# Kernel optimization log

Hardware: AMD Instinct MI355X
Metric: run time of the kernel (lower is better)

Reference implementation:

```python
import jax, jax.numpy as jnp
import numpy as np

B, S, D = 4, 8192, 512


def setup_inputs() -> dict:
    key = jax.random.key(0)
    k1, k2, k3 = jax.random.split(key, 3)
    input_real = jax.random.normal(k1, (B, S, D), dtype=jnp.float32)
    input_imag = jax.random.normal(k2, (B, S, D), dtype=jnp.float32)
    weight = jax.random.uniform(k3, (B, S), dtype=jnp.float32)
    return {"input_real": input_real, "input_imag": input_imag, "weight": weight}


def reference(input_real, input_imag, weight):
    # Original: sum_s w[b,s] * (r_s r_s^T + i_s i_s^T)  and  sum_s w[b,s] * (i_s r_s^T - r_s i_s^T).
    # Algebraically equal to weighted Gram GEMMs X^T diag(w) Y; avoids the [B,S,D,D] intermediate.
    def wgram(x, y):
        # [B,S,D] x [B,S] x [B,S,D] -> [B,D,D]
        return jnp.einsum('bsd,bs,bse->bde', x, weight, y)

    output_r = wgram(input_real, input_real) + wgram(input_imag, input_imag)
    output_i = wgram(input_imag, input_real) - wgram(input_real, input_imag)
    return (output_r, output_i)
```

## Files before the change

### kernel.cpp

```cpp
#include <hip/hip_runtime.h>
#include <cstdint>
#include <cstddef>

#define NB 4
#define NS 8192
#define ND 512
#define NP 1024
#define BK 32

typedef __bf16 bf16x8 __attribute__((ext_vector_type(8)));
typedef float f32x4 __attribute__((ext_vector_type(4)));

union FragU { uint4 u; bf16x8 h; };

__device__ __forceinline__ void gload16(const void* g, void* l) {
  __builtin_amdgcn_global_load_lds(
      (const __attribute__((address_space(1))) unsigned int*)g,
      (__attribute__((address_space(3))) unsigned int*)l, 16, 0, 0);
}

__global__ __launch_bounds__(256)
void k_prep(const float* __restrict__ R, const float* __restrict__ I,
            const float* __restrict__ W, unsigned short* __restrict__ Yt) {
  __shared__ unsigned T[64][34];
  const int t   = threadIdx.x;
  const int blk = blockIdx.x;
  const int sb  = blk & 127;
  const int pb  = (blk >> 7) & 15;
  const int b   = blk >> 11;
  const float* src = (pb < 8) ? R : I;
  const int col0 = (pb & 7) * 64;
  const int s0 = sb * 64;
  const int c2 = t & 15;
  const int rp = t >> 4;
#pragma unroll
  for (int i = 0; i < 2; ++i) {
    const int r  = rp + 16 * i;
    const int sa = s0 + 2 * r;
    const float swa = sqrtf(W[b * NS + sa]);
    const float swb = sqrtf(W[b * NS + sa + 1]);
    const float4 va = *(const float4*)(src + (size_t)(b * NS + sa) * ND + col0 + c2 * 4);
    const float4 vb = *(const float4*)(src + (size_t)(b * NS + sa + 1) * ND + col0 + c2 * 4);
    unsigned p0, p1, p2, p3;
    asm("v_cvt_pk_bf16_f32 %0, %1, %2" : "=v"(p0) : "v"(va.x * swa), "v"(vb.x * swb));
    asm("v_cvt_pk_bf16_f32 %0, %1, %2" : "=v"(p1) : "v"(va.y * swa), "v"(vb.y * swb));
    asm("v_cvt_pk_bf16_f32 %0, %1, %2" : "=v"(p2) : "v"(va.z * swa), "v"(vb.z * swb));
    asm("v_cvt_pk_bf16_f32 %0, %1, %2" : "=v"(p3) : "v"(va.w * swa), "v"(vb.w * swb));
    T[c2 * 4 + 0][r] = p0;
    T[c2 * 4 + 1][r] = p1;
    T[c2 * 4 + 2][r] = p2;
    T[c2 * 4 + 3][r] = p3;
  }
  __syncthreads();
  const int sc = t & 7;
  const int d0 = t >> 3;
#pragma unroll
  for (int i = 0; i < 2; ++i) {
    const int d = d0 + 32 * i;
    uint4 o;
    o.x = T[d][sc * 4 + 0];
    o.y = T[d][sc * 4 + 1];
    o.z = T[d][sc * 4 + 2];
    o.w = T[d][sc * 4 + 3];
    *(uint4*)(Yt + (size_t)(b * NP + pb * 64 + d) * NS + s0 + sc * 8) = o;
  }
}

__global__ __launch_bounds__(256, 2)
void k_gemm(const unsigned short* __restrict__ Yt, float* __restrict__ part) {
  __shared__ uint4 lds4[4096];
  char* lds = (char*)lds4;
  static const int TMp[10] = {0,1,1,2,2,2,3,3,3,3};
  static const int TNp[10] = {0,0,1,0,1,2,0,1,2,3};
  const int j  = blockIdx.x;
  const int g0 = j * 20;
  const int g1 = g0 + 20;
  const int p0 = g0 >> 8;
  const int p1 = (g1 - 1) >> 8;
  const int t = threadIdx.x;
  const int l = t & 63, w = t >> 6;

  const int cj = l & 7, jj = l >> 3;
  const int ec = cj ^ jj;
  const int rbase = w * 16 + 2 * jj + (ec >> 2);
  const int colo  = (ec & 3) * 8;
  int dstoff[8];
#pragma unroll
  for (int u = 0; u < 8; ++u) dstoff[u] = (u >> 1) * 8192 + (u & 1) * 4096 + w * 1024;

  const int gfr = l >> 4, e_ = l & 1, q = (l >> 1) & 7;
  const int ibase = ((l & 15) >> 1) * 128 + ((64 * e_ + 16 * gfr) ^ (q << 4));
  const int wm = w & 1, wn = w >> 1;
  const int mfb = wm * 4096, nfb = wn * 4096;
  const int lr = (l >> 4) * 4, lc = l & 15;

  for (int seg = 0; seg < 2; ++seg) {
    int pos, k0, ns;
    if (seg == 0) {
      pos = p0; k0 = g0 & 255;
      ns = 256 - k0; if (ns > 20) ns = 20;
    } else {
      if (p1 == p0) break;
      pos = p1; k0 = 0; ns = g1 & 255;
    }
    const int b = pos / 10, p = pos % 10;
    const int tm = TMp[p], tn = TNp[p];
    const int prow[4] = { tm * 128, 512 + tm * 128, tn * 128, 512 + tn * 128 };
    const unsigned short* gsrc[8];
#pragma unroll
    for (int u = 0; u < 8; ++u)
      gsrc[u] = Yt + (size_t)(b * NP + prow[u >> 1] + (u & 1) * 64 + rbase) * NS
                + (size_t)k0 * BK + colo;

    f32x4 accr[4][4], acci[4][4];
    const f32x4 zz = {0.f, 0.f, 0.f, 0.f};
#pragma unroll
    for (int a = 0; a < 4; ++a)
#pragma unroll
      for (int c = 0; c < 4; ++c) { accr[a][c] = zz; acci[a][c] = zz; }

#pragma unroll
    for (int u = 0; u < 8; ++u) { gload16(gsrc[u], lds + dstoff[u]); gsrc[u] += BK; }
    __builtin_amdgcn_sched_barrier(0);
    asm volatile("s_waitcnt vmcnt(0)" ::: "memory");
    __builtin_amdgcn_s_barrier();

    int cur = 0;
    for (int ks = 0; ks < ns; ++ks) {
      const int cbase = cur * 32768;
      if (ks + 1 < ns) {
        const int nbase = cbase ^ 32768;
#pragma unroll
        for (int u = 0; u < 8; ++u) { gload16(gsrc[u], lds + nbase + dstoff[u]); gsrc[u] += BK; }
        __builtin_amdgcn_sched_barrier(0);
        asm volatile("s_waitcnt vmcnt(8)" ::: "memory");
      } else {
        asm volatile("s_waitcnt vmcnt(0)" ::: "memory");
      }
      __builtin_amdgcn_s_barrier();

      FragU ar[4], ai[4];
#pragma unroll
      for (int mf = 0; mf < 4; ++mf) {
        ar[mf].u = *(const uint4*)(lds + cbase +        mfb + mf * 1024 + ibase);
        ai[mf].u = *(const uint4*)(lds + cbase + 8192 + mfb + mf * 1024 + ibase);
      }
      __builtin_amdgcn_s_setprio(1);
#pragma unroll
      for (int nf = 0; nf < 4; ++nf) {
        FragU br, bi, bin;
        br.u = *(const uint4*)(lds + cbase + 16384 + nfb + nf * 1024 + ibase);
        bi.u = *(const uint4*)(lds + cbase + 24576 + nfb + nf * 1024 + ibase);
        bin.u.x = bi.u.x ^ 0x80008000u;
        bin.u.y = bi.u.y ^ 0x80008000u;
        bin.u.z = bi.u.z ^ 0x80008000u;
        bin.u.w = bi.u.w ^ 0x80008000u;
#pragma unroll
        for (int mf = 0; mf < 4; ++mf) {
          accr[mf][nf] = __builtin_amdgcn_mfma_f32_16x16x32_bf16(ar[mf].h, br.h,  accr[mf][nf], 0, 0, 0);
          accr[mf][nf] = __builtin_amdgcn_mfma_f32_16x16x32_bf16(ai[mf].h, bi.h,  accr[mf][nf], 0, 0, 0);
          acci[mf][nf] = __builtin_amdgcn_mfma_f32_16x16x32_bf16(ai[mf].h, br.h,  acci[mf][nf], 0, 0, 0);
          acci[mf][nf] = __builtin_amdgcn_mfma_f32_16x16x32_bf16(ar[mf].h, bin.h, acci[mf][nf], 0, 0, 0);
        }
      }
      __builtin_amdgcn_s_setprio(0);
      __builtin_amdgcn_s_barrier();
      cur ^= 1;
    }

    const int slot = (seg == 0) ? j : (512 + pos);
    const size_t baser = (size_t)slot * 32768;
    const size_t basei = baser + 16384;
#pragma unroll
    for (int mf = 0; mf < 4; ++mf)
#pragma unroll
      for (int nf = 0; nf < 4; ++nf)
#pragma unroll
        for (int r = 0; r < 4; ++r) {
          const int mi = wm * 64 + mf * 16 + lr + r;
          const int ni = wn * 64 + nf * 16 + lc;
          part[baser + (size_t)mi * 128 + ni] = accr[mf][nf][r];
          part[basei + (size_t)mi * 128 + ni] = acci[mf][nf][r];
        }
  }
}

__global__ __launch_bounds__(256)
void k_reduce(const float* __restrict__ part, float* __restrict__ out) {
  static const int TMp[10] = {0,1,1,2,2,2,3,3,3,3};
  static const int TNp[10] = {0,0,1,0,1,2,0,1,2,3};
  const int idx = blockIdx.x * 256 + threadIdx.x;
  const int ni = idx & 127;
  const int mi = (idx >> 7) & 127;
  const int o  = (idx >> 14) & 1;
  const int P  = idx >> 15;
  const int jlo = (256 * P + 19) / 20;
  const int jhi = (256 * P + 255) / 20;
  const size_t off = (size_t)o * 16384 + (size_t)mi * 128 + ni;
  float a = 0.f;
  for (int s = jlo; s <= jhi; ++s)
    a += part[(size_t)s * 32768 + off];
  if ((256 * P) % 20)
    a += part[(size_t)(512 + P) * 32768 + off];
  const int b = P / 10, p = P % 10;
  const int d = TMp[p] * 128 + mi;
  const int e = TNp[p] * 128 + ni;
  out[(size_t)o * 1048576 + (size_t)b * 262144 + (size_t)d * 512 + e] = a;
}

__global__ __launch_bounds__(256)
void k_mirror(float* __restrict__ out) {
  __shared__ float T[64][65];
  static const int UM[6] = {0,0,0,1,1,2};
  static const int UN[6] = {1,2,3,2,3,3};
  const int m = blockIdx.x;
  const int sub = m & 3;
  const int b   = (m >> 2) & 3;
  const int o   = (m >> 4) & 1;
  const int u   = m >> 5;
  const int d0 = UM[u] * 128 + (sub & 1) * 64;
  const int e0 = UN[u] * 128 + ((sub >> 1) & 1) * 64;
  const float sign = o ? -1.f : 1.f;
  float* base = out + (size_t)o * 1048576 + (size_t)b * 262144;
  const int t  = threadIdx.x;
  const int c4 = (t & 15) * 4;
  const int r0 = t >> 4;
#pragma unroll
  for (int i = 0; i < 4; ++i) {
    const int r = r0 + i * 16;
    const float4 v = *(const float4*)(base + (size_t)(e0 + r) * 512 + d0 + c4);
    T[c4 + 0][r] = v.x; T[c4 + 1][r] = v.y;
    T[c4 + 2][r] = v.z; T[c4 + 3][r] = v.w;
  }
  __syncthreads();
#pragma unroll
  for (int i = 0; i < 4; ++i) {
    const int r = r0 + i * 16;
    float4 wv;
    wv.x = sign * T[r][c4 + 0]; wv.y = sign * T[r][c4 + 1];
    wv.z = sign * T[r][c4 + 2]; wv.w = sign * T[r][c4 + 3];
    *(float4*)(base + (size_t)(d0 + r) * 512 + e0 + c4) = wv;
  }
}

__global__ __launch_bounds__(256)
void k_fallback(const float* __restrict__ R, const float* __restrict__ I,
                const float* __restrict__ W, float* __restrict__ out) {
  __shared__ float Rd[64][32], Id[64][32], Re[64][32], Ie[64][32];
  const int blk = blockIdx.x;
  const int et = blk & 15, dt = (blk >> 4) & 15, b = blk >> 8;
  const int d0 = dt * 32, e0 = et * 32;
  const int t = threadIdx.x;
  const int dd = t >> 3;
  const int ee0 = (t & 7) * 4;
  float ar[4] = {0,0,0,0}, ai[4] = {0,0,0,0};
  for (int s0 = 0; s0 < NS; s0 += 64) {
#pragma unroll
    for (int k = 0; k < 8; ++k) {
      const int idx = t + k * 256;
      const int row = idx >> 5, col = idx & 31;
      const float sw = sqrtf(W[b * NS + s0 + row]);
      const size_t gr = (size_t)(b * NS + s0 + row) * ND;
      Rd[row][col] = R[gr + d0 + col] * sw;
      Id[row][col] = I[gr + d0 + col] * sw;
      Re[row][col] = R[gr + e0 + col] * sw;
      Ie[row][col] = I[gr + e0 + col] * sw;
    }
    __syncthreads();
    for (int s = 0; s < 64; ++s) {
      const float rd = Rd[s][dd], id = Id[s][dd];
#pragma unroll
      for (int jx = 0; jx < 4; ++jx) {
        const float re = Re[s][ee0 + jx], ie = Ie[s][ee0 + jx];
        ar[jx] += rd * re + id * ie;
        ai[jx] += id * re - rd * ie;
      }
    }
    __syncthreads();
  }
  const size_t ob = (size_t)b * 262144;
#pragma unroll
  for (int jx = 0; jx < 4; ++jx) {
    out[          ob + (size_t)(d0 + dd) * 512 + e0 + ee0 + jx] = ar[jx];
    out[1048576 + ob + (size_t)(d0 + dd) * 512 + e0 + ee0 + jx] = ai[jx];
  }
}

extern "C" void kernel_launch(void* const* d_in, const int* in_sizes, int n_in,
                              void* d_out, int out_size, void* d_ws, size_t ws_size,
                              hipStream_t stream) {
  const float* R = (const float*)d_in[0];
  const float* I = (const float*)d_in[1];
  const float* W = (const float*)d_in[2];
  float* out = (float*)d_out;
  const size_t ytBytes   = (size_t)NB * NP * NS * 2;
  const size_t partBytes = (size_t)552 * 32768 * 4;

  if (ws_size < ytBytes + partBytes) {
    k_fallback<<<dim3(NB * 16 * 16), dim3(256), 0, stream>>>(R, I, W, out);
    return;
  }

  unsigned short* Yt = (unsigned short*)d_ws;
  float* part = (float*)((char*)d_ws + ytBytes);

  k_prep<<<dim3(NB * 16 * 128), dim3(256), 0, stream>>>(R, I, W, Yt);
  k_gemm<<<dim3(512), dim3(256), 0, stream>>>(Yt, part);
  k_reduce<<<dim3(5120), dim3(256), 0, stream>>>(part, out);
  k_mirror<<<dim3(192), dim3(256), 0, stream>>>(out);
}
```

Before: 232.6 us.

## Use 8-wave GEMM blocks, swizzle block order, vectorize partial reduction

The GEMM kernel now runs 512 threads per block. Each wave owns a 32x64 sub-tile instead of 64x64, which halves its accumulator registers and the global-to-LDS loads per thread. Block indices are remapped so that consecutive blocks land on strided work chunks, likely for better spread across XCDs or cache locality. The reduction kernel now reads and writes float4 instead of scalars and launches a quarter as many blocks. The trade-off is more LDS fragment reads per MFMA for each wave and higher register pressure from the launch_bounds(512,4) target.

```diff
diff --git a/kernel.cpp b/kernel.cpp
--- a/kernel.cpp
+++ b/kernel.cpp
@@ -66,13 +66,14 @@
   }
 }
 
-__global__ __launch_bounds__(256, 2)
+__global__ __launch_bounds__(512, 4)
 void k_gemm(const unsigned short* __restrict__ Yt, float* __restrict__ part) {
   __shared__ uint4 lds4[4096];
   char* lds = (char*)lds4;
   static const int TMp[10] = {0,1,1,2,2,2,3,3,3,3};
   static const int TNp[10] = {0,0,1,0,1,2,0,1,2,3};
-  const int j  = blockIdx.x;
+  const int bid = blockIdx.x;
+  const int j   = (bid & 7) * 64 + (bid >> 3);
   const int g0 = j * 20;
   const int g1 = g0 + 20;
   const int p0 = g0 >> 8;
@@ -84,14 +85,15 @@
   const int ec = cj ^ jj;
   const int rbase = w * 16 + 2 * jj + (ec >> 2);
   const int colo  = (ec & 3) * 8;
-  int dstoff[8];
-#pragma unroll
-  for (int u = 0; u < 8; ++u) dstoff[u] = (u >> 1) * 8192 + (u & 1) * 4096 + w * 1024;
+  int dstoff[4];
+#pragma unroll
+  for (int u = 0; u < 4; ++u) dstoff[u] = u * 8192 + w * 1024;
 
   const int gfr = l >> 4, e_ = l & 1, q = (l >> 1) & 7;
   const int ibase = ((l & 15) >> 1) * 128 + ((64 * e_ + 16 * gfr) ^ (q << 4));
-  const int wm = w & 1, wn = w >> 1;
-  const int mfb = wm * 4096, nfb = wn * 4096;
+  const int wm = w & 3, wn = w >> 2;
+  const int mfb = wm * 2048;
+  const int nfb = wn * 4096;
   const int lr = (l >> 4) * 4, lc = l & 15;
 
   for (int seg = 0; seg < 2; ++seg) {
@@ -106,21 +108,21 @@
     const int b = pos / 10, p = pos % 10;
     const int tm = TMp[p], tn = TNp[p];
     const int prow[4] = { tm * 128, 512 + tm * 128, tn * 128, 512 + tn * 128 };
-    const unsigned short* gsrc[8];
-#pragma unroll
-    for (int u = 0; u < 8; ++u)
-      gsrc[u] = Yt + (size_t)(b * NP + prow[u >> 1] + (u & 1) * 64 + rbase) * NS
+    const unsigned short* gsrc[4];
+#pragma unroll
+    for (int u = 0; u < 4; ++u)
+      gsrc[u] = Yt + (size_t)(b * NP + prow[u] + rbase) * NS
                 + (size_t)k0 * BK + colo;
 
-    f32x4 accr[4][4], acci[4][4];
+    f32x4 accr[2][4], acci[2][4];
     const f32x4 zz = {0.f, 0.f, 0.f, 0.f};
 #pragma unroll
-    for (int a = 0; a < 4; ++a)
+    for (int a = 0; a < 2; ++a)
 #pragma unroll
       for (int c = 0; c < 4; ++c) { accr[a][c] = zz; acci[a][c] = zz; }
 
 #pragma unroll
-    for (int u = 0; u < 8; ++u) { gload16(gsrc[u], lds + dstoff[u]); gsrc[u] += BK; }
+    for (int u = 0; u < 4; ++u) { gload16(gsrc[u], lds + dstoff[u]); gsrc[u] += BK; }
     __builtin_amdgcn_sched_barrier(0);
     asm volatile("s_waitcnt vmcnt(0)" ::: "memory");
     __builtin_amdgcn_s_barrier();
@@ -131,17 +133,17 @@
       if (ks + 1 < ns) {
         const int nbase = cbase ^ 32768;
 #pragma unroll
-        for (int u = 0; u < 8; ++u) { gload16(gsrc[u], lds + nbase + dstoff[u]); gsrc[u] += BK; }
+        for (int u = 0; u < 4; ++u) { gload16(gsrc[u], lds + nbase + dstoff[u]); gsrc[u] += BK; }
         __builtin_amdgcn_sched_barrier(0);
-        asm volatile("s_waitcnt vmcnt(8)" ::: "memory");
+        asm volatile("s_waitcnt vmcnt(4)" ::: "memory");
       } else {
         asm volatile("s_waitcnt vmcnt(0)" ::: "memory");
       }
       __builtin_amdgcn_s_barrier();
 
-      FragU ar[4], ai[4];
-#pragma unroll
-      for (int mf = 0; mf < 4; ++mf) {
+      FragU ar[2], ai[2];
+#pragma unroll
+      for (int mf = 0; mf < 2; ++mf) {
         ar[mf].u = *(const uint4*)(lds + cbase +        mfb + mf * 1024 + ibase);
         ai[mf].u = *(const uint4*)(lds + cbase + 8192 + mfb + mf * 1024 + ibase);
       }
@@ -156,7 +158,7 @@
         bin.u.z = bi.u.z ^ 0x80008000u;
         bin.u.w = bi.u.w ^ 0x80008000u;
 #pragma unroll
-        for (int mf = 0; mf < 4; ++mf) {
+        for (int mf = 0; mf < 2; ++mf) {
           accr[mf][nf] = __builtin_amdgcn_mfma_f32_16x16x32_bf16(ar[mf].h, br.h,  accr[mf][nf], 0, 0, 0);
           accr[mf][nf] = __builtin_amdgcn_mfma_f32_16x16x32_bf16(ai[mf].h, bi.h,  accr[mf][nf], 0, 0, 0);
           acci[mf][nf] = __builtin_amdgcn_mfma_f32_16x16x32_bf16(ai[mf].h, br.h,  acci[mf][nf], 0, 0, 0);
@@ -172,12 +174,12 @@
     const size_t baser = (size_t)slot * 32768;
     const size_t basei = baser + 16384;
 #pragma unroll
-    for (int mf = 0; mf < 4; ++mf)
+    for (int mf = 0; mf < 2; ++mf)
 #pragma unroll
       for (int nf = 0; nf < 4; ++nf)
 #pragma unroll
         for (int r = 0; r < 4; ++r) {
-          const int mi = wm * 64 + mf * 16 + lr + r;
+          const int mi = wm * 32 + mf * 16 + lr + r;
           const int ni = wn * 64 + nf * 16 + lc;
           part[baser + (size_t)mi * 128 + ni] = accr[mf][nf][r];
           part[basei + (size_t)mi * 128 + ni] = acci[mf][nf][r];
@@ -190,22 +192,27 @@
   static const int TMp[10] = {0,1,1,2,2,2,3,3,3,3};
   static const int TNp[10] = {0,0,1,0,1,2,0,1,2,3};
   const int idx = blockIdx.x * 256 + threadIdx.x;
-  const int ni = idx & 127;
-  const int mi = (idx >> 7) & 127;
-  const int o  = (idx >> 14) & 1;
-  const int P  = idx >> 15;
+  const int n4 = idx & 31;
+  const int mi = (idx >> 5) & 127;
+  const int o  = (idx >> 12) & 1;
+  const int P  = idx >> 13;
   const int jlo = (256 * P + 19) / 20;
   const int jhi = (256 * P + 255) / 20;
-  const size_t off = (size_t)o * 16384 + (size_t)mi * 128 + ni;
-  float a = 0.f;
-  for (int s = jlo; s <= jhi; ++s)
-    a += part[(size_t)s * 32768 + off];
-  if ((256 * P) % 20)
-    a += part[(size_t)(512 + P) * 32768 + off];
+  const size_t off = (size_t)o * 16384 + (size_t)mi * 128 + n4 * 4;
+  float4 a = {0.f, 0.f, 0.f, 0.f};
+  for (int s = jlo; s <= jhi; ++s) {
+    const float4 v = *(const float4*)(part + (size_t)s * 32768 + off);
+    a.x += v.x; a.y += v.y; a.z += v.z; a.w += v.w;
+  }
+  if ((256 * P) % 20) {
+    const float4 v = *(const float4*)(part + (size_t)(512 + P) * 32768 + off);
+    a.x += v.x; a.y += v.y; a.z += v.z; a.w += v.w;
+  }
   const int b = P / 10, p = P % 10;
   const int d = TMp[p] * 128 + mi;
-  const int e = TNp[p] * 128 + ni;
-  out[(size_t)o * 1048576 + (size_t)b * 262144 + (size_t)d * 512 + e] = a;
+  const int e = TNp[p] * 128 + n4 * 4;
+  *(float4*)(out + (size_t)o * 1048576 + (size_t)b * 262144
+             + (size_t)d * 512 + e) = a;
 }
 
 __global__ __launch_bounds__(256)
@@ -305,7 +312,7 @@
   float* part = (float*)((char*)d_ws + ytBytes);
 
   k_prep<<<dim3(NB * 16 * 128), dim3(256), 0, stream>>>(R, I, W, Yt);
-  k_gemm<<<dim3(512), dim3(256), 0, stream>>>(Yt, part);
-  k_reduce<<<dim3(5120), dim3(256), 0, stream>>>(part, out);
+  k_gemm<<<dim3(512), dim3(512), 0, stream>>>(Yt, part);
+  k_reduce<<<dim3(1280), dim3(256), 0, stream>>>(part, out);
   k_mirror<<<dim3(192), dim3(256), 0, stream>>>(out);
 }
```

Result: no change. 229.0 us (-1.5%).
